# Kernel tuning notes

Measured on AMD Instinct MI355X. Metric: run time of the kernel, lower is better.

The kernel has to match this reference:

```python
import jax, jax.numpy as jnp
import numpy as np
from math import sqrt

B, S, D, H = 2, 2048, 1024, 16
HD = D // H


def setup_inputs() -> dict:
    key = jax.random.key(0)
    ks = jax.random.split(key, 5)
    std = 0.02
    return {
        "tensor_in": jax.random.normal(ks[0], (B, S, D), dtype=jnp.float32),
        "attention_mask": jnp.zeros((1, 1, S, S), dtype=jnp.float32),
        "Wq": jax.random.normal(ks[1], (D, D), dtype=jnp.float32) * std,
        "Wk": jax.random.normal(ks[2], (D, D), dtype=jnp.float32) * std,
        "Wv": jax.random.normal(ks[3], (D, D), dtype=jnp.float32) * std,
        "Wo": jax.random.normal(ks[4], (D, D), dtype=jnp.float32) * std,
    }


def reference(tensor_in, attention_mask, Wq, Wk, Wv, Wo):
    # nn.Linear(dim, dim, bias=False): y = x @ W.T, W is [out, in]
    q = tensor_in @ Wq.T  # [B,S,D]
    k = tensor_in @ Wk.T
    v = tensor_in @ Wv.T
    # split heads -> [B,H,S,HD]
    q = q.reshape(B, S, H, HD).transpose(0, 2, 1, 3)
    k = k.reshape(B, S, H, HD).transpose(0, 2, 1, 3)
    v = v.reshape(B, S, H, HD).transpose(0, 2, 1, 3)
    # scores [B,H,S,S]; note: mask added BEFORE scaling, scale = sqrt(full dim)
    scores = jnp.einsum("bhqd,bhkd->bhqk", q, k) + attention_mask
    weights = jax.nn.softmax(scores / sqrt(D), axis=-1)  # dropout = identity (eval)
    context = jnp.einsum("bhqk,bhkd->bhqd", weights, v)
    context = context.transpose(0, 2, 1, 3).reshape(B, S, D)
    return context @ Wo.T
```

## Files before the change

### kernel.cpp

```cpp
#include <hip/hip_runtime.h>

#define B_  2
#define S_  2048
#define D_  1024
#define H_  16
#define HD_ 64
#define M_  (B_*S_)

typedef __attribute__((ext_vector_type(8))) short  short8;
typedef __attribute__((ext_vector_type(4))) float  float4v;
typedef __attribute__((ext_vector_type(4))) int    int4v;
typedef __attribute__((ext_vector_type(4))) unsigned short ushort4v;

#define QSCALE 0.03125f

__device__ __forceinline__ unsigned short f_to_bf16bits(float f) {
    unsigned int x = __builtin_bit_cast(unsigned int, f);
    unsigned int lsb = (x >> 16) & 1u;
    x += 0x7fffu + lsb;
    return (unsigned short)(x >> 16);
}

__device__ __forceinline__ void async16(unsigned short* lds, const unsigned short* g) {
    __builtin_amdgcn_global_load_lds(
        (const __attribute__((address_space(1))) void*)g,
        (__attribute__((address_space(3))) void*)lds, 16, 0, 0);
}

__global__ __launch_bounds__(256) void cvt_bf16(
    const float* __restrict__ X,  const float* __restrict__ Wq,
    const float* __restrict__ Wk, const float* __restrict__ Wv,
    const float* __restrict__ Wo,
    unsigned short* __restrict__ Xb,  unsigned short* __restrict__ Wqb,
    unsigned short* __restrict__ Wkb, unsigned short* __restrict__ Wvb,
    unsigned short* __restrict__ Wob)
{
    const long t = (long)blockIdx.x * 256 + threadIdx.x;
    const long e = t * 8;
    const float* src; unsigned short* dst; long off;
    if      (e < 4194304) { src = X;  dst = Xb;  off = e; }
    else if (e < 5242880) { src = Wq; dst = Wqb; off = e - 4194304; }
    else if (e < 6291456) { src = Wk; dst = Wkb; off = e - 5242880; }
    else if (e < 7340032) { src = Wv; dst = Wvb; off = e - 6291456; }
    else                  { src = Wo; dst = Wob; off = e - 7340032; }
    float4v a = *(const float4v*)&src[off];
    float4v b = *(const float4v*)&src[off + 4];
    int4v o;
    o[0] = (int)f_to_bf16bits(a[0]) | ((int)f_to_bf16bits(a[1]) << 16);
    o[1] = (int)f_to_bf16bits(a[2]) | ((int)f_to_bf16bits(a[3]) << 16);
    o[2] = (int)f_to_bf16bits(b[0]) | ((int)f_to_bf16bits(b[1]) << 16);
    o[3] = (int)f_to_bf16bits(b[2]) | ((int)f_to_bf16bits(b[3]) << 16);
    *(int4v*)&dst[off] = o;
}

__global__ __launch_bounds__(256) void gemm_bt(
    const unsigned short* __restrict__ A,
    const unsigned short* __restrict__ B0,
    const unsigned short* __restrict__ B1,
    const unsigned short* __restrict__ B2,
    void* __restrict__ O0, void* __restrict__ O1, void* __restrict__ O2,
    int mode_base)
{
    const int K = 1024;
    const int z = blockIdx.z;
    const int mode = mode_base + z;
    const unsigned short* Aop;
    const unsigned short* Bop;
    void* Op = (z == 0) ? O0 : (z == 1) ? O1 : O2;
    int m0, n0;
    if (mode == 2) {
        Aop = B2; Bop = A;
        m0 = blockIdx.y * 128;
        n0 = blockIdx.x * 128;
    } else {
        Aop = A;
        Bop = (z == 0) ? B0 : (z == 1) ? B1 : B2;
        m0 = blockIdx.x * 128;
        n0 = blockIdx.y * 128;
    }

    __shared__ alignas(16) unsigned short As[128 * 32];
    __shared__ alignas(16) unsigned short Bs[128 * 32];

    const int tid  = threadIdx.x;
    const int wv   = tid >> 6;
    const int lane = tid & 63;
    const int wm   = wv >> 1, wn = wv & 1;
    const int q4   = lane >> 4, l15 = lane & 15;

    const int r0 = (wv * 2 + 0) * 16 + (lane >> 2);
    const int r1 = (wv * 2 + 1) * 16 + (lane >> 2);
    const int c0 = (((lane & 3) ^ (r0 & 3)) * 8);
    const int c1 = (((lane & 3) ^ (r1 & 3)) * 8);
    const unsigned short* gA0 = Aop + (long)(m0 + r0) * K + c0;
    const unsigned short* gA1 = Aop + (long)(m0 + r1) * K + c1;
    const unsigned short* gB0 = Bop + (long)(n0 + r0) * K + c0;
    const unsigned short* gB1 = Bop + (long)(n0 + r1) * K + c1;
    const int slot0 = (wv * 2 + 0) * 512;
    const int slot1 = (wv * 2 + 1) * 512;

    const int swz = (q4 ^ (l15 & 3)) * 8;
    int aoff[4], boff[4];
#pragma unroll
    for (int t = 0; t < 4; t++) {
        aoff[t] = (wm * 64 + t * 16 + l15) * 32 + swz;
        boff[t] = (wn * 64 + t * 16 + l15) * 32 + swz;
    }

    float4v acc[4][4];
#pragma unroll
    for (int i = 0; i < 4; i++)
#pragma unroll
        for (int j = 0; j < 4; j++) acc[i][j] = (float4v)0.0f;

    for (int k0 = 0; k0 < K; k0 += 32) {
        __syncthreads();
        async16(&As[slot0], gA0); async16(&As[slot1], gA1);
        async16(&Bs[slot0], gB0); async16(&Bs[slot1], gB1);
        gA0 += 32; gA1 += 32; gB0 += 32; gB1 += 32;
        __syncthreads();

        short8 afr[4], bfr[4];
#pragma unroll
        for (int mt = 0; mt < 4; mt++) afr[mt] = *(const short8*)&As[aoff[mt]];
#pragma unroll
        for (int nt = 0; nt < 4; nt++) bfr[nt] = *(const short8*)&Bs[boff[nt]];
#pragma unroll
        for (int mt = 0; mt < 4; mt++)
#pragma unroll
            for (int nt = 0; nt < 4; nt++)
                acc[mt][nt] = __builtin_amdgcn_mfma_f32_16x16x32_bf16(
                    afr[mt], bfr[nt], acc[mt][nt], 0, 0, 0);
    }

#pragma unroll
    for (int mt = 0; mt < 4; mt++)
#pragma unroll
        for (int nt = 0; nt < 4; nt++)
#pragma unroll
            for (int r = 0; r < 4; r++) {
                const int m = m0 + wm * 64 + mt * 16 + q4 * 4 + r;
                const int n = n0 + wn * 64 + nt * 16 + l15;
                float v = acc[mt][nt][r];
                if (mode == 3) {
                    ((float*)Op)[(long)m * D_ + n] = v;
                } else if (mode == 2) {
                    const long off = (((long)(n >> 11) * H_ + (m >> 6)) * HD_ + (m & 63)) * S_ + (n & 2047);
                    ((unsigned short*)Op)[off] = f_to_bf16bits(v);
                } else {
                    const long off = ((long)((m >> 11) * H_ + (n >> 6)) * S_ + (m & 2047)) * HD_ + (n & 63);
                    if (mode == 0) v *= QSCALE;
                    ((unsigned short*)Op)[off] = f_to_bf16bits(v);
                }
            }
}

__global__ __launch_bounds__(256) void attn(
    const unsigned short* __restrict__ Q,
    const unsigned short* __restrict__ Kk,
    const unsigned short* __restrict__ Vt,
    const float* __restrict__ mask,
    unsigned short* __restrict__ ctx)
{
    __shared__ alignas(16) unsigned short KV[2][2][64 * 64];
    __shared__ alignas(16) unsigned short Ps[4][16 * 64];

    const int tid  = threadIdx.x;
    const int wv   = tid >> 6;
    const int lane = tid & 63;
    const int q4   = lane >> 4, l15 = lane & 15;
    const int bh   = blockIdx.y;
    const int q0   = blockIdx.x * 64;

    const long head = (long)bh * S_ * HD_;

    const int qrow = q0 + wv * 16 + l15;
    short8 qfr[2];
    qfr[0] = *(const short8*)&Q[head + (long)qrow * HD_ + q4 * 8];
    qfr[1] = *(const short8*)&Q[head + (long)qrow * HD_ + 32 + q4 * 8];

    float l_acc[4];
#pragma unroll
    for (int r = 0; r < 4; r++) l_acc[r] = 0.0f;
    float4v oacc[4];
#pragma unroll
    for (int dt = 0; dt < 4; dt++) oacc[dt] = (float4v)0.0f;

    const int srow = lane >> 3;
    const int sch  = lane & 7;
    const int row0 = wv * 16 + srow;
    const int row1 = wv * 16 + 8 + srow;
    const int cc0  = ((sch ^ (row0 & 7)) * 8);
    const int cc1  = ((sch ^ (row1 & 7)) * 8);
    const unsigned short* gK0 = Kk + head + (long)row0 * HD_ + cc0;
    const unsigned short* gK1 = Kk + head + (long)row1 * HD_ + cc1;
    const unsigned short* gV0 = Vt + head + (long)row0 * S_  + cc0;
    const unsigned short* gV1 = Vt + head + (long)row1 * S_  + cc1;
    const int ldsK0 = (wv * 16 + 0) * 64;
    const int ldsK1 = (wv * 16 + 8) * 64;

    const float* mrow[4];
#pragma unroll
    for (int r = 0; r < 4; r++)
        mrow[r] = mask + (long)(q0 + wv * 16 + q4 * 4 + r) * S_ + l15;

    async16(&KV[0][0][ldsK0], gK0);
    async16(&KV[0][0][ldsK1], gK1);
    async16(&KV[0][1][ldsK0], gV0);
    async16(&KV[0][1][ldsK1], gV1);
    float mv[4][4];
#pragma unroll
    for (int nt = 0; nt < 4; nt++)
#pragma unroll
        for (int r = 0; r < 4; r++) mv[nt][r] = mrow[r][nt * 16];

    const int pswz = (q4 & 1) * 4;
    const int psl3 = l15 >> 3;

    for (int k0 = 0; k0 < S_; k0 += 64) {
        const int buf = (k0 >> 6) & 1;
        __syncthreads();

        if (k0 + 64 < S_) {
            async16(&KV[buf ^ 1][0][ldsK0], gK0 + (long)(k0 + 64) * HD_);
            async16(&KV[buf ^ 1][0][ldsK1], gK1 + (long)(k0 + 64) * HD_);
            async16(&KV[buf ^ 1][1][ldsK0], gV0 + (k0 + 64));
            async16(&KV[buf ^ 1][1][ldsK1], gV1 + (k0 + 64));
        }

        float4v sfr[4];
#pragma unroll
        for (int nt = 0; nt < 4; nt++) {
            const int row = nt * 16 + l15;
            const int p0 = ((q4     ^ (row & 7)) * 8);
            const int p1 = (((4+q4) ^ (row & 7)) * 8);
            short8 kb0 = *(const short8*)&KV[buf][0][row * 64 + p0];
            short8 kb1 = *(const short8*)&KV[buf][0][row * 64 + p1];
            float4v s = (float4v)0.0f;
            s = __builtin_amdgcn_mfma_f32_16x16x32_bf16(qfr[0], kb0, s, 0, 0, 0);
            s = __builtin_amdgcn_mfma_f32_16x16x32_bf16(qfr[1], kb1, s, 0, 0, 0);
            sfr[nt] = s;
        }

        float mvn[4][4];
        const int knext = (k0 + 64 < S_) ? k0 + 64 : k0;
#pragma unroll
        for (int nt = 0; nt < 4; nt++)
#pragma unroll
            for (int r = 0; r < 4; r++) mvn[nt][r] = mrow[r][knext + nt * 16];

#pragma unroll
        for (int nt = 0; nt < 4; nt++)
#pragma unroll
            for (int r = 0; r < 4; r++) {
                const float p = __expf(fmaf(mv[nt][r], QSCALE, sfr[nt][r]));
                l_acc[r] += p;
                const int c8 = (nt * 2 + psl3) ^ (pswz + r);
                Ps[wv][(q4 * 4 + r) * 64 + c8 * 8 + (l15 & 7)] = f_to_bf16bits(p);
            }

        const int pp0 = ((q4     ^ (l15 & 7)) * 8);
        const int pp1 = (((4+q4) ^ (l15 & 7)) * 8);
        short8 pf0 = *(const short8*)&Ps[wv][l15 * 64 + pp0];
        short8 pf1 = *(const short8*)&Ps[wv][l15 * 64 + pp1];

#pragma unroll
        for (int dt = 0; dt < 4; dt++) {
            const int row = dt * 16 + l15;
            const int p0 = ((q4     ^ (row & 7)) * 8);
            const int p1 = (((4+q4) ^ (row & 7)) * 8);
            short8 vb0 = *(const short8*)&KV[buf][1][row * 64 + p0];
            short8 vb1 = *(const short8*)&KV[buf][1][row * 64 + p1];
            float4v o = oacc[dt];
            o = __builtin_amdgcn_mfma_f32_16x16x32_bf16(pf0, vb0, o, 0, 0, 0);
            o = __builtin_amdgcn_mfma_f32_16x16x32_bf16(pf1, vb1, o, 0, 0, 0);
            oacc[dt] = o;
        }

#pragma unroll
        for (int nt = 0; nt < 4; nt++)
#pragma unroll
            for (int r = 0; r < 4; r++) mv[nt][r] = mvn[nt][r];
    }

#pragma unroll
    for (int r = 0; r < 4; r++) {
#pragma unroll
        for (int off = 1; off < 16; off <<= 1)
            l_acc[r] += __shfl_xor(l_acc[r], off);
    }

    const int b = bh >> 4, h = bh & 15;
#pragma unroll
    for (int dt = 0; dt < 4; dt++)
#pragma unroll
        for (int r = 0; r < 4; r++) {
            const int qg = q0 + wv * 16 + q4 * 4 + r;
            const int d  = dt * 16 + l15;
            const float v = oacc[dt][r] / l_acc[r];
            ctx[((long)(b * S_ + qg)) * D_ + h * HD_ + d] = f_to_bf16bits(v);
        }
}

extern "C" void kernel_launch(void* const* d_in, const int* in_sizes, int n_in,
                              void* d_out, int out_size, void* d_ws, size_t ws_size,
                              hipStream_t stream) {
    const float* X    = (const float*)d_in[0];
    const float* mask = (const float*)d_in[1];
    const float* Wq   = (const float*)d_in[2];
    const float* Wk   = (const float*)d_in[3];
    const float* Wv   = (const float*)d_in[4];
    const float* Wo   = (const float*)d_in[5];
    float* out        = (float*)d_out;

    unsigned short* ws = (unsigned short*)d_ws;
    unsigned short* qws  = ws;
    unsigned short* kws  = ws + 4194304;
    unsigned short* vtws = ws + 8388608;
    unsigned short* ctx  = ws + 12582912;
    unsigned short* Xb   = ws + 16777216;
    unsigned short* Wqb  = ws + 20971520;
    unsigned short* Wkb  = ws + 22020096;
    unsigned short* Wvb  = ws + 23068672;
    unsigned short* Wob  = ws + 24117248;

    cvt_bf16<<<dim3(4096), 256, 0, stream>>>(X, Wq, Wk, Wv, Wo, Xb, Wqb, Wkb, Wvb, Wob);
    gemm_bt<<<dim3(32, 8, 3), 256, 0, stream>>>(Xb, Wqb, Wkb, Wvb, qws, kws, vtws, 0);
    attn<<<dim3(32, 32, 1), 256, 0, stream>>>(qws, kws, vtws, mask, ctx);
    gemm_bt<<<dim3(32, 8, 1), 256, 0, stream>>>(ctx, Wob, Wob, Wob, out, out, out, 3);
}
```

Measured before the change: 259.9 us.

## Deepen GEMM K-tile to 64 and use register-prefetch K/V staging in attention

The projection GEMM now stages 64-wide K slices per iteration, with an 8-chunk XOR swizzle, and runs two MFMA sub-steps per barrier pair. This halves the number of synchronisation rounds and doubles the bytes in flight per load phase. The attention kernel drops the async LDS double buffer: it prefetches the next K/V tile into registers, then writes it into a single LDS buffer behind an extra barrier. It also swaps which grid axis indexes heads and which indexes query blocks, changing block scheduling order. The trade-offs are more LDS per GEMM block, an added barrier, and register staging in attention.

```diff
diff --git a/kernel.cpp b/kernel.cpp
--- a/kernel.cpp
+++ b/kernel.cpp
@@ -79,8 +79,8 @@
         n0 = blockIdx.y * 128;
     }
 
-    __shared__ alignas(16) unsigned short As[128 * 32];
-    __shared__ alignas(16) unsigned short Bs[128 * 32];
+    __shared__ alignas(16) unsigned short As[128 * 64];
+    __shared__ alignas(16) unsigned short Bs[128 * 64];
 
     const int tid  = threadIdx.x;
     const int wv   = tid >> 6;
@@ -88,24 +88,27 @@
     const int wm   = wv >> 1, wn = wv & 1;
     const int q4   = lane >> 4, l15 = lane & 15;
 
-    const int r0 = (wv * 2 + 0) * 16 + (lane >> 2);
-    const int r1 = (wv * 2 + 1) * 16 + (lane >> 2);
-    const int c0 = (((lane & 3) ^ (r0 & 3)) * 8);
-    const int c1 = (((lane & 3) ^ (r1 & 3)) * 8);
-    const unsigned short* gA0 = Aop + (long)(m0 + r0) * K + c0;
-    const unsigned short* gA1 = Aop + (long)(m0 + r1) * K + c1;
-    const unsigned short* gB0 = Bop + (long)(n0 + r0) * K + c0;
-    const unsigned short* gB1 = Bop + (long)(n0 + r1) * K + c1;
-    const int slot0 = (wv * 2 + 0) * 512;
-    const int slot1 = (wv * 2 + 1) * 512;
-
-    const int swz = (q4 ^ (l15 & 3)) * 8;
-    int aoff[4], boff[4];
-#pragma unroll
-    for (int t = 0; t < 4; t++) {
-        aoff[t] = (wm * 64 + t * 16 + l15) * 32 + swz;
-        boff[t] = (wn * 64 + t * 16 + l15) * 32 + swz;
-    }
+    const unsigned short* gA[4];
+    const unsigned short* gB[4];
+    int slotj[4];
+#pragma unroll
+    for (int j = 0; j < 4; j++) {
+        const int r = wv * 32 + j * 8 + (lane >> 3);
+        const int c = (((lane & 7) ^ (r & 7)) * 8);
+        gA[j] = Aop + (long)(m0 + r) * K + c;
+        gB[j] = Bop + (long)(n0 + r) * K + c;
+        slotj[j] = (wv * 32 + j * 8) * 64;
+    }
+
+    int aoff[2][4], boff[2][4];
+#pragma unroll
+    for (int ks = 0; ks < 2; ks++)
+#pragma unroll
+        for (int t = 0; t < 4; t++) {
+            const int swz = (((ks * 4 + q4) ^ (l15 & 7)) * 8);
+            aoff[ks][t] = (wm * 64 + t * 16 + l15) * 64 + swz;
+            boff[ks][t] = (wn * 64 + t * 16 + l15) * 64 + swz;
+        }
 
     float4v acc[4][4];
 #pragma unroll
@@ -113,24 +116,30 @@
 #pragma unroll
         for (int j = 0; j < 4; j++) acc[i][j] = (float4v)0.0f;
 
-    for (int k0 = 0; k0 < K; k0 += 32) {
+    for (int k0 = 0; k0 < K; k0 += 64) {
         __syncthreads();
-        async16(&As[slot0], gA0); async16(&As[slot1], gA1);
-        async16(&Bs[slot0], gB0); async16(&Bs[slot1], gB1);
-        gA0 += 32; gA1 += 32; gB0 += 32; gB1 += 32;
+#pragma unroll
+        for (int j = 0; j < 4; j++) {
+            async16(&As[slotj[j]], gA[j]);
+            async16(&Bs[slotj[j]], gB[j]);
+            gA[j] += 64; gB[j] += 64;
+        }
         __syncthreads();
 
-        short8 afr[4], bfr[4];
-#pragma unroll
-        for (int mt = 0; mt < 4; mt++) afr[mt] = *(const short8*)&As[aoff[mt]];
-#pragma unroll
-        for (int nt = 0; nt < 4; nt++) bfr[nt] = *(const short8*)&Bs[boff[nt]];
-#pragma unroll
-        for (int mt = 0; mt < 4; mt++)
-#pragma unroll
-            for (int nt = 0; nt < 4; nt++)
-                acc[mt][nt] = __builtin_amdgcn_mfma_f32_16x16x32_bf16(
-                    afr[mt], bfr[nt], acc[mt][nt], 0, 0, 0);
+#pragma unroll
+        for (int ks = 0; ks < 2; ks++) {
+            short8 afr[4], bfr[4];
+#pragma unroll
+            for (int mt = 0; mt < 4; mt++) afr[mt] = *(const short8*)&As[aoff[ks][mt]];
+#pragma unroll
+            for (int nt = 0; nt < 4; nt++) bfr[nt] = *(const short8*)&Bs[boff[ks][nt]];
+#pragma unroll
+            for (int mt = 0; mt < 4; mt++)
+#pragma unroll
+                for (int nt = 0; nt < 4; nt++)
+                    acc[mt][nt] = __builtin_amdgcn_mfma_f32_16x16x32_bf16(
+                        afr[mt], bfr[nt], acc[mt][nt], 0, 0, 0);
+        }
     }
 
 #pragma unroll
@@ -162,15 +171,16 @@
     const float* __restrict__ mask,
     unsigned short* __restrict__ ctx)
 {
-    __shared__ alignas(16) unsigned short KV[2][2][64 * 64];
+    __shared__ alignas(16) unsigned short Ks[64 * 64];
+    __shared__ alignas(16) unsigned short Vs[64 * 64];
     __shared__ alignas(16) unsigned short Ps[4][16 * 64];
 
     const int tid  = threadIdx.x;
     const int wv   = tid >> 6;
     const int lane = tid & 63;
     const int q4   = lane >> 4, l15 = lane & 15;
-    const int bh   = blockIdx.y;
-    const int q0   = blockIdx.x * 64;
+    const int bh   = blockIdx.x;
+    const int q0   = blockIdx.y * 64;
 
     const long head = (long)bh * S_ * HD_;
 
@@ -186,28 +196,24 @@
 #pragma unroll
     for (int dt = 0; dt < 4; dt++) oacc[dt] = (float4v)0.0f;
 
-    const int srow = lane >> 3;
-    const int sch  = lane & 7;
-    const int row0 = wv * 16 + srow;
-    const int row1 = wv * 16 + 8 + srow;
-    const int cc0  = ((sch ^ (row0 & 7)) * 8);
-    const int cc1  = ((sch ^ (row1 & 7)) * 8);
-    const unsigned short* gK0 = Kk + head + (long)row0 * HD_ + cc0;
-    const unsigned short* gK1 = Kk + head + (long)row1 * HD_ + cc1;
-    const unsigned short* gV0 = Vt + head + (long)row0 * S_  + cc0;
-    const unsigned short* gV1 = Vt + head + (long)row1 * S_  + cc1;
-    const int ldsK0 = (wv * 16 + 0) * 64;
-    const int ldsK1 = (wv * 16 + 8) * 64;
+    const int row0 = tid >> 3, row1 = row0 + 32, sch = tid & 7;
+    const int cc   = ((sch ^ (row0 & 7)) * 8);
+    const unsigned short* gK0 = Kk + head + (long)row0 * HD_ + cc;
+    const unsigned short* gK1 = Kk + head + (long)row1 * HD_ + cc;
+    const unsigned short* gV0 = Vt + head + (long)row0 * S_  + cc;
+    const unsigned short* gV1 = Vt + head + (long)row1 * S_  + cc;
+    const int ldsOff0 = row0 * 64 + sch * 8;
+    const int ldsOff1 = row1 * 64 + sch * 8;
 
     const float* mrow[4];
 #pragma unroll
     for (int r = 0; r < 4; r++)
         mrow[r] = mask + (long)(q0 + wv * 16 + q4 * 4 + r) * S_ + l15;
 
-    async16(&KV[0][0][ldsK0], gK0);
-    async16(&KV[0][0][ldsK1], gK1);
-    async16(&KV[0][1][ldsK0], gV0);
-    async16(&KV[0][1][ldsK1], gV1);
+    int4v kr0 = *(const int4v*)gK0;
+    int4v kr1 = *(const int4v*)gK1;
+    int4v vr0 = *(const int4v*)gV0;
+    int4v vr1 = *(const int4v*)gV1;
     float mv[4][4];
 #pragma unroll
     for (int nt = 0; nt < 4; nt++)
@@ -218,24 +224,28 @@
     const int psl3 = l15 >> 3;
 
     for (int k0 = 0; k0 < S_; k0 += 64) {
-        const int buf = (k0 >> 6) & 1;
         __syncthreads();
+        *(int4v*)&Ks[ldsOff0] = kr0;
+        *(int4v*)&Ks[ldsOff1] = kr1;
+        *(int4v*)&Vs[ldsOff0] = vr0;
+        *(int4v*)&Vs[ldsOff1] = vr1;
+        __syncthreads();
 
         if (k0 + 64 < S_) {
-            async16(&KV[buf ^ 1][0][ldsK0], gK0 + (long)(k0 + 64) * HD_);
-            async16(&KV[buf ^ 1][0][ldsK1], gK1 + (long)(k0 + 64) * HD_);
-            async16(&KV[buf ^ 1][1][ldsK0], gV0 + (k0 + 64));
-            async16(&KV[buf ^ 1][1][ldsK1], gV1 + (k0 + 64));
+            kr0 = *(const int4v*)(gK0 + (long)(k0 + 64) * HD_);
+            kr1 = *(const int4v*)(gK1 + (long)(k0 + 64) * HD_);
+            vr0 = *(const int4v*)(gV0 + (k0 + 64));
+            vr1 = *(const int4v*)(gV1 + (k0 + 64));
         }
 
         float4v sfr[4];
 #pragma unroll
         for (int nt = 0; nt < 4; nt++) {
             const int row = nt * 16 + l15;
-            const int p0 = ((q4     ^ (row & 7)) * 8);
-            const int p1 = (((4+q4) ^ (row & 7)) * 8);
-            short8 kb0 = *(const short8*)&KV[buf][0][row * 64 + p0];
-            short8 kb1 = *(const short8*)&KV[buf][0][row * 64 + p1];
+            const int p0 = ((q4       ^ (row & 7)) * 8);
+            const int p1 = (((4 + q4) ^ (row & 7)) * 8);
+            short8 kb0 = *(const short8*)&Ks[row * 64 + p0];
+            short8 kb1 = *(const short8*)&Ks[row * 64 + p1];
             float4v s = (float4v)0.0f;
             s = __builtin_amdgcn_mfma_f32_16x16x32_bf16(qfr[0], kb0, s, 0, 0, 0);
             s = __builtin_amdgcn_mfma_f32_16x16x32_bf16(qfr[1], kb1, s, 0, 0, 0);
@@ -259,18 +269,18 @@
                 Ps[wv][(q4 * 4 + r) * 64 + c8 * 8 + (l15 & 7)] = f_to_bf16bits(p);
             }
 
-        const int pp0 = ((q4     ^ (l15 & 7)) * 8);
-        const int pp1 = (((4+q4) ^ (l15 & 7)) * 8);
+        const int pp0 = ((q4       ^ (l15 & 7)) * 8);
+        const int pp1 = (((4 + q4) ^ (l15 & 7)) * 8);
         short8 pf0 = *(const short8*)&Ps[wv][l15 * 64 + pp0];
         short8 pf1 = *(const short8*)&Ps[wv][l15 * 64 + pp1];
 
 #pragma unroll
         for (int dt = 0; dt < 4; dt++) {
             const int row = dt * 16 + l15;
-            const int p0 = ((q4     ^ (row & 7)) * 8);
-            const int p1 = (((4+q4) ^ (row & 7)) * 8);
-            short8 vb0 = *(const short8*)&KV[buf][1][row * 64 + p0];
-            short8 vb1 = *(const short8*)&KV[buf][1][row * 64 + p1];
+            const int p0 = ((q4       ^ (row & 7)) * 8);
+            const int p1 = (((4 + q4) ^ (row & 7)) * 8);
+            short8 vb0 = *(const short8*)&Vs[row * 64 + p0];
+            short8 vb1 = *(const short8*)&Vs[row * 64 + p1];
             float4v o = oacc[dt];
             o = __builtin_amdgcn_mfma_f32_16x16x32_bf16(pf0, vb0, o, 0, 0, 0);
             o = __builtin_amdgcn_mfma_f32_16x16x32_bf16(pf1, vb1, o, 0, 0, 0);
```

New measurement: 244.8 us. 5.8% less time.
